# Kernel tuning notes

Measured on AMD Instinct MI355X. Metric: run time of the kernel, lower is better.

The kernel has to match this reference:

```python
import jax, jax.numpy as jnp
import numpy as np

FEATURE_SIZE = 1_000_000
EMB = 64
BATCH = 16384
ONEHOT = 26
MULTIHOT = 2
MH_LEN = 20
DENSE = 13
NN_IN = EMB * (ONEHOT + MULTIHOT) + DENSE  # 1805
UNITS = [1024, 512, 1]


def setup_inputs() -> dict:
    key = jax.random.key(0)
    ks = jax.random.split(key, 12)
    glorot = lambda k, shape: jax.random.normal(k, shape, jnp.float32) * np.sqrt(2.0 / (shape[0] + shape[-1])).astype(np.float32)
    return {
        "dense": jax.random.normal(ks[0], (BATCH, DENSE), jnp.float32),
        "onehot": jax.random.randint(ks[1], (BATCH, ONEHOT), 0, FEATURE_SIZE),
        "multihot": jax.random.randint(ks[2], (BATCH, MULTIHOT, MH_LEN), 0, FEATURE_SIZE),
        "fm_w": glorot(ks[3], (FEATURE_SIZE, 1)),
        "fm_emb": glorot(ks[4], (FEATURE_SIZE, EMB)),
        "w0": glorot(ks[5], (NN_IN, UNITS[0])),
        "b0": jnp.zeros((1,), jnp.float32),
        "w1": glorot(ks[6], (UNITS[0], UNITS[1])),
        "b1": jnp.zeros((1,), jnp.float32),
        "w2": glorot(ks[7], (UNITS[1], UNITS[2])),
        "b2": jnp.zeros((1,), jnp.float32),
    }


def reference(dense, onehot, multihot, fm_w, fm_emb, w0, b0, w1, b1, w2, b2):
    B = dense.shape[0]
    # Embedding gathers
    onehot_emb = fm_emb[onehot]                       # (B, 26, E)
    multihot_emb = fm_emb[multihot].mean(axis=2)      # (B, 2, L, E) -> (B, 2, E) mean combiner
    cat_emb = jnp.concatenate([onehot_emb, multihot_emb], axis=1)  # (B, 28, E)
    # FM 1st order (only onehot, as in original code)
    fm_1st = jnp.sum(fm_w[onehot], axis=1)            # (B, 1)
    # FM 2nd order: 0.5 * ((sum v)^2 - sum v^2)
    s = jnp.sum(cat_emb, axis=1)                      # (B, E)
    fm_2nd = 0.5 * (jnp.square(s) - jnp.sum(jnp.square(cat_emb), axis=1))
    fm_2nd = jnp.sum(fm_2nd, axis=1, keepdims=True)   # (B, 1)
    # Deep part (ReLU on every layer, incl. last, as in original)
    nn = jnp.concatenate([cat_emb.reshape(B, -1), dense], axis=1)  # (B, 1805)
    for w, b in ((w0, b0), (w1, b1), (w2, b2)):
        nn = jax.nn.relu(nn @ w + b)
    return jax.nn.sigmoid(fm_1st + fm_2nd + nn)       # (B, 1)
```

## Files before the change

### kernel.cpp

```cpp
#include <hip/hip_runtime.h>
#include <hip/hip_bf16.h>
#include <math.h>

typedef __attribute__((ext_vector_type(8))) short bf16x8;
typedef __attribute__((ext_vector_type(4))) float f32x4;

typedef void __attribute__((address_space(1))) gvoid_t;
typedef void __attribute__((address_space(3))) lvoid_t;

#define KP0   1824
#define NB    16384
#define OFF_X    0u
#define OFF_H0   59768832u
#define OFF_W0T  93323264u
#define OFF_W1T  97058816u
#define OFF_FM   98107392u

#define VMCNT(n) asm volatile("s_waitcnt vmcnt(" #n ")" ::: "memory")

__device__ __forceinline__ float bf2f(short s) {
    return __uint_as_float(((unsigned)(unsigned short)s) << 16);
}

__device__ __forceinline__ void load_lds16(const void* g, void* l) {
    __builtin_amdgcn_global_load_lds(
        (gvoid_t*)(uintptr_t)g,
        (lvoid_t*)(unsigned)(uintptr_t)l,
        16, 0, 0);
}

__global__ __launch_bounds__(256) void transpose_w(const float* __restrict__ W,
                                                   __hip_bfloat16* __restrict__ WT,
                                                   int K, int N, int KP) {
    __shared__ float tile[32][33];
    const int k0 = blockIdx.x * 32, n0 = blockIdx.y * 32;
    const int tx = threadIdx.x, ty = threadIdx.y;
    #pragma unroll
    for (int i = 0; i < 32; i += 8) {
        int k = k0 + ty + i;
        tile[ty + i][tx] = (k < K) ? W[(size_t)k * N + (n0 + tx)] : 0.f;
    }
    __syncthreads();
    #pragma unroll
    for (int i = 0; i < 32; i += 8) {
        int n = n0 + ty + i, k = k0 + tx;
        WT[(size_t)n * KP + k] = __float2bfloat16(tile[tx][ty + i]);
    }
}

__global__ __launch_bounds__(256) void gather_fm(const float* __restrict__ dense,
                                                 const int* __restrict__ onehot,
                                                 const int* __restrict__ multihot,
                                                 const float* __restrict__ fm_w,
                                                 const float* __restrict__ fm_emb,
                                                 __hip_bfloat16* __restrict__ X,
                                                 float* __restrict__ FM) {
    const int wv = threadIdx.x >> 6, lane = threadIdx.x & 63;
    const int row = blockIdx.x * 4 + wv;
    const int oh = (lane < 26) ? onehot[row * 26 + lane] : 0;
    const int mh = (lane < 40) ? multihot[row * 40 + lane] : 0;
    const float fm1 = (lane < 26) ? fm_w[oh] : 0.f;
    __hip_bfloat16* Xr = X + (size_t)row * KP0;
    float s = 0.f, sq = 0.f;
    for (int f = 0; f < 26; ++f) {
        int idx = __shfl(oh, f);
        float v = fm_emb[(size_t)idx * 64 + lane];
        s += v; sq += v * v;
        Xr[f * 64 + lane] = __float2bfloat16(v);
    }
    #pragma unroll
    for (int h = 0; h < 2; ++h) {
        float a = 0.f;
        for (int l = 0; l < 20; ++l) {
            int idx = __shfl(mh, h * 20 + l);
            a += fm_emb[(size_t)idx * 64 + lane];
        }
        float v = a * (1.f / 20.f);
        s += v; sq += v * v;
        Xr[(26 + h) * 64 + lane] = __float2bfloat16(v);
    }
    float red = 0.5f * (s * s - sq) + fm1;
    #pragma unroll
    for (int off = 32; off; off >>= 1) red += __shfl_xor(red, off);
    if (lane == 0) FM[row] = red;
    if (lane < 32) {
        float dv = (lane < 13) ? dense[row * 13 + lane] : 0.f;
        Xr[1792 + lane] = __float2bfloat16(dv);
    }
}

template<int NREP>
__global__ __launch_bounds__(512, 2) void gemm_pipe(const __hip_bfloat16* __restrict__ A,
                                                    const __hip_bfloat16* __restrict__ BT,
                                                    const float* __restrict__ bias,
                                                    __hip_bfloat16* __restrict__ C,
                                                    int M, int N, int K) {
    constexpr int BBY = NREP * 4096;
    __shared__ __align__(16) char lds[4][16384 + BBY];
    const int tid = threadIdx.x;
    const int wv = tid >> 6, lane = tid & 63;
    const int lr = lane & 15, lg = lane >> 4;
    const int wr = wv >> 2, wc = wv & 3;

    const int bid = blockIdx.x;
    const int wg = (bid & 7) * 32 + (bid >> 3);
    const int br = wg >> 2, bc = wg & 3;

    const size_t rowBytes = (size_t)K * 2;
    const char* Ab = (const char*)A + (size_t)(br * 256) * rowBytes;
    const char* Bb = (const char*)BT + (size_t)(bc * (NREP * 64)) * rowBytes;
    const int nt = K >> 5;

    auto stage = [&](int kt) {
        const int buf = kt & 3;
        const size_t kb = (size_t)kt * 64;
        #pragma unroll
        for (int i = 0; i < 2; ++i) {
            int o = i * 8192 + wv * 1024 + lane * 16;
            int row = o >> 6, slot = (o >> 4) & 3;
            int sg = slot ^ ((row >> 1) & 3);
            load_lds16(Ab + (size_t)row * rowBytes + kb + sg * 16,
                       &lds[buf][i * 8192 + wv * 1024]);
        }
        #pragma unroll
        for (int i = 0; i < NREP / 2; ++i) {
            int o = i * 8192 + wv * 1024 + lane * 16;
            int row = o >> 6, slot = (o >> 4) & 3;
            int sg = slot ^ ((row >> 1) & 3);
            load_lds16(Bb + (size_t)row * rowBytes + kb + sg * 16,
                       &lds[buf][16384 + i * 8192 + wv * 1024]);
        }
    };

    f32x4 acc[8][NREP] = {};

    stage(0); stage(1); stage(2);
    if constexpr (NREP == 4) VMCNT(8); else VMCNT(6);
    __builtin_amdgcn_s_barrier();
    __builtin_amdgcn_sched_barrier(0);

    const int swz = ((lr >> 1) & 3) << 4;
    const int aoff0 = (wr * 128 + lr) * 64 + ((lg << 4) ^ swz);
    const int boff0 = 16384 + (wc * (NREP * 16) + lr) * 64 + ((lg << 4) ^ swz);

    for (int kt = 0; kt < nt; ++kt) {
        if (kt + 3 < nt) stage(kt + 3);
        __builtin_amdgcn_sched_barrier(0);

        const char* base = lds[kt & 3];
        bf16x8 a[8], b[NREP];
        #pragma unroll
        for (int m = 0; m < 8; ++m)
            a[m] = *(const bf16x8*)(base + aoff0 + m * 1024);
        #pragma unroll
        for (int n = 0; n < NREP; ++n)
            b[n] = *(const bf16x8*)(base + boff0 + n * 1024);

        __builtin_amdgcn_s_setprio(1);
        #pragma unroll
        for (int m = 0; m < 8; ++m)
            #pragma unroll
            for (int n = 0; n < NREP; ++n)
                acc[m][n] = __builtin_amdgcn_mfma_f32_16x16x32_bf16(a[m], b[n], acc[m][n], 0, 0, 0);
        __builtin_amdgcn_s_setprio(0);

        if (kt + 1 < nt) {
            asm volatile("s_waitcnt lgkmcnt(0)" ::: "memory");
            if (kt + 3 < nt)      { if constexpr (NREP == 4) VMCNT(8); else VMCNT(6); }
            else if (kt + 2 < nt) { if constexpr (NREP == 4) VMCNT(4); else VMCNT(3); }
            else                  { VMCNT(0); }
            __builtin_amdgcn_s_barrier();
            __builtin_amdgcn_sched_barrier(0);
        }
    }

    const float bv = bias[0];
    const int rowb = br * 256 + wr * 128, colb = bc * (NREP * 64) + wc * (NREP * 16);
    #pragma unroll
    for (int m = 0; m < 8; ++m)
        #pragma unroll
        for (int n = 0; n < NREP; ++n)
            #pragma unroll
            for (int r = 0; r < 4; ++r) {
                int row = rowb + m * 16 + lg * 4 + r;
                int col = colb + n * 16 + lr;
                C[(size_t)row * N + col] = __float2bfloat16(fmaxf(acc[m][n][r] + bv, 0.f));
            }
}

__global__ __launch_bounds__(256) void final_k(const __hip_bfloat16* __restrict__ H1,
                                               const float* __restrict__ w2,
                                               const float* __restrict__ b2,
                                               const float* __restrict__ FM,
                                               float* __restrict__ out) {
    const int wv = threadIdx.x >> 6, lane = threadIdx.x & 63;
    const int row = blockIdx.x * 4 + wv;
    const bf16x8 h = *(const bf16x8*)(H1 + (size_t)row * 512 + lane * 8);
    float s = 0.f;
    #pragma unroll
    for (int j = 0; j < 8; ++j) s += bf2f(h[j]) * w2[lane * 8 + j];
    #pragma unroll
    for (int off = 32; off; off >>= 1) s += __shfl_xor(s, off);
    if (lane == 0) {
        float v = fmaxf(s + b2[0], 0.f) + FM[row];
        out[row] = 1.f / (1.f + expf(-v));
    }
}

extern "C" void kernel_launch(void* const* d_in, const int* in_sizes, int n_in,
                              void* d_out, int out_size, void* d_ws, size_t ws_size,
                              hipStream_t stream) {
    const float* dense    = (const float*)d_in[0];
    const int*   onehot   = (const int*)d_in[1];
    const int*   multihot = (const int*)d_in[2];
    const float* fm_w     = (const float*)d_in[3];
    const float* fm_emb   = (const float*)d_in[4];
    const float* w0       = (const float*)d_in[5];
    const float* b0       = (const float*)d_in[6];
    const float* w1       = (const float*)d_in[7];
    const float* b1       = (const float*)d_in[8];
    const float* w2       = (const float*)d_in[9];
    const float* b2       = (const float*)d_in[10];
    float* out = (float*)d_out;

    char* ws = (char*)d_ws;
    __hip_bfloat16* X   = (__hip_bfloat16*)(ws + OFF_X);
    __hip_bfloat16* H1  = (__hip_bfloat16*)(ws + OFF_X);
    __hip_bfloat16* H0  = (__hip_bfloat16*)(ws + OFF_H0);
    __hip_bfloat16* W0T = (__hip_bfloat16*)(ws + OFF_W0T);
    __hip_bfloat16* W1T = (__hip_bfloat16*)(ws + OFF_W1T);
    float*          FM  = (float*)(ws + OFF_FM);

    transpose_w<<<dim3(57, 32), dim3(32, 8), 0, stream>>>(w0, W0T, 1805, 1024, KP0);
    transpose_w<<<dim3(32, 16), dim3(32, 8), 0, stream>>>(w1, W1T, 1024, 512, 1024);
    gather_fm<<<NB / 4, 256, 0, stream>>>(dense, onehot, multihot, fm_w, fm_emb, X, FM);
    gemm_pipe<4><<<256, 512, 0, stream>>>(X,  W0T, b0, H0, NB, 1024, KP0);
    gemm_pipe<2><<<256, 512, 0, stream>>>(H0, W1T, b1, H1, NB, 512, 1024);
    final_k<<<NB / 4, 256, 0, stream>>>(H1, w2, b2, FM, out);
}
```

Baseline: 178.0 us.

## Restructure GEMM to 64-wide K tiles with padded LDS and interleaved staging

The GEMM kernel now uses 64-element K tiles in a double-buffered LDS layout with padded rows (144/160 bytes) instead of an XOR swizzle and a 4-deep 32-wide pipeline. Each K step is split into phases, and global-to-LDS loads for tile t+2 are interleaved between MFMA phases, with a barrier around each phase. KP0 is raised to 1856 so K is a multiple of 64, and workspace offsets and the gather padding are adjusted to match. The aim is fewer loop iterations and better overlap of loads with MFMA, at the cost of many more barriers and some extra zero-padded K work.

```diff
diff --git a/kernel.cpp b/kernel.cpp
--- a/kernel.cpp
+++ b/kernel.cpp
@@ -8,15 +8,17 @@
 typedef void __attribute__((address_space(1))) gvoid_t;
 typedef void __attribute__((address_space(3))) lvoid_t;
 
-#define KP0   1824
+#define KP0   1856
 #define NB    16384
 #define OFF_X    0u
-#define OFF_H0   59768832u
-#define OFF_W0T  93323264u
-#define OFF_W1T  97058816u
-#define OFF_FM   98107392u
+#define OFF_H0   60817408u
+#define OFF_W0T  94371840u
+#define OFF_W1T  98172928u
+#define OFF_FM   99221504u
 
 #define VMCNT(n) asm volatile("s_waitcnt vmcnt(" #n ")" ::: "memory")
+#define LGKM0()  asm volatile("s_waitcnt lgkmcnt(0)" ::: "memory")
+#define SBAR0()  __builtin_amdgcn_sched_barrier(0)
 
 __device__ __forceinline__ float bf2f(short s) {
     return __uint_as_float(((unsigned)(unsigned short)s) << 16);
@@ -83,10 +85,8 @@
     #pragma unroll
     for (int off = 32; off; off >>= 1) red += __shfl_xor(red, off);
     if (lane == 0) FM[row] = red;
-    if (lane < 32) {
-        float dv = (lane < 13) ? dense[row * 13 + lane] : 0.f;
-        Xr[1792 + lane] = __float2bfloat16(dv);
-    }
+    float dv = (lane < 13) ? dense[row * 13 + lane] : 0.f;
+    Xr[1792 + lane] = __float2bfloat16(dv);
 }
 
 template<int NREP>
@@ -95,8 +95,13 @@
                                                     const float* __restrict__ bias,
                                                     __hip_bfloat16* __restrict__ C,
                                                     int M, int N, int K) {
-    constexpr int BBY = NREP * 4096;
-    __shared__ __align__(16) char lds[4][16384 + BBY];
+    constexpr int AB   = 256 * 144;
+    constexpr int BROW = (NREP == 4) ? 144 : 160;
+    constexpr int BB   = (NREP == 4) ? 256 * 144 : 128 * 160;
+    constexpr int TOT  = AB + BB;
+    constexpr int LOADS = TOT / 8192;
+    __shared__ __align__(16) char lds[2][TOT];
+
     const int tid = threadIdx.x;
     const int wv = tid >> 6, lane = tid & 63;
     const int lr = lane & 15, lg = lane >> 4;
@@ -109,69 +114,152 @@
     const size_t rowBytes = (size_t)K * 2;
     const char* Ab = (const char*)A + (size_t)(br * 256) * rowBytes;
     const char* Bb = (const char*)BT + (size_t)(bc * (NREP * 64)) * rowBytes;
-    const int nt = K >> 5;
-
-    auto stage = [&](int kt) {
-        const int buf = kt & 3;
-        const size_t kb = (size_t)kt * 64;
-        #pragma unroll
-        for (int i = 0; i < 2; ++i) {
-            int o = i * 8192 + wv * 1024 + lane * 16;
-            int row = o >> 6, slot = (o >> 4) & 3;
-            int sg = slot ^ ((row >> 1) & 3);
-            load_lds16(Ab + (size_t)row * rowBytes + kb + sg * 16,
-                       &lds[buf][i * 8192 + wv * 1024]);
-        }
-        #pragma unroll
-        for (int i = 0; i < NREP / 2; ++i) {
-            int o = i * 8192 + wv * 1024 + lane * 16;
-            int row = o >> 6, slot = (o >> 4) & 3;
-            int sg = slot ^ ((row >> 1) & 3);
-            load_lds16(Bb + (size_t)row * rowBytes + kb + sg * 16,
-                       &lds[buf][16384 + i * 8192 + wv * 1024]);
-        }
+    const int nt = K >> 6;
+
+    auto stage_chunk = [&](int t, int i) {
+        const size_t kb = (size_t)t * 128;
+        const int o = i * 8192 + tid * 16;
+        const char* src;
+        if (o < AB) {
+            int row = o / 144, c = o % 144;
+            if (c >= 128) c = 0;
+            src = Ab + (size_t)row * rowBytes + kb + c;
+        } else {
+            int ob = o - AB;
+            int row = ob / BROW, c = ob % BROW;
+            if (c >= 128) c = 0;
+            src = Bb + (size_t)row * rowBytes + kb + c;
+        }
+        load_lds16(src, &lds[t & 1][i * 8192 + wv * 1024]);
     };
 
     f32x4 acc[8][NREP] = {};
 
-    stage(0); stage(1); stage(2);
-    if constexpr (NREP == 4) VMCNT(8); else VMCNT(6);
+    for (int i = 0; i < LOADS; ++i) stage_chunk(0, i);
+    for (int i = 0; i < LOADS; ++i) stage_chunk(1, i);
+    if constexpr (NREP == 4) VMCNT(9); else VMCNT(7);
     __builtin_amdgcn_s_barrier();
-    __builtin_amdgcn_sched_barrier(0);
-
-    const int swz = ((lr >> 1) & 3) << 4;
-    const int aoff0 = (wr * 128 + lr) * 64 + ((lg << 4) ^ swz);
-    const int boff0 = 16384 + (wc * (NREP * 16) + lr) * 64 + ((lg << 4) ^ swz);
-
-    for (int kt = 0; kt < nt; ++kt) {
-        if (kt + 3 < nt) stage(kt + 3);
-        __builtin_amdgcn_sched_barrier(0);
-
-        const char* base = lds[kt & 3];
-        bf16x8 a[8], b[NREP];
-        #pragma unroll
-        for (int m = 0; m < 8; ++m)
-            a[m] = *(const bf16x8*)(base + aoff0 + m * 1024);
-        #pragma unroll
-        for (int n = 0; n < NREP; ++n)
-            b[n] = *(const bf16x8*)(base + boff0 + n * 1024);
-
+    SBAR0();
+
+    const int aoff = (wr * 128 + lr) * 144 + lg * 16;
+    const int boff = AB + (wc * (NREP * 16) + lr) * BROW + lg * 16;
+
+    for (int t = 0; t < nt; ++t) {
+        const char* L = &lds[t & 1][0];
+        const bool st = (t + 2 < nt);
+        bf16x8 a[4][2], b[NREP][2];
+
+        #pragma unroll
+        for (int m = 0; m < 4; ++m)
+            #pragma unroll
+            for (int kk = 0; kk < 2; ++kk)
+                a[m][kk] = *(const bf16x8*)(L + aoff + m * 2304 + kk * 64);
+        #pragma unroll
+        for (int n = 0; n < 2; ++n)
+            #pragma unroll
+            for (int kk = 0; kk < 2; ++kk)
+                b[n][kk] = *(const bf16x8*)(L + boff + n * (16 * BROW) + kk * 64);
+        SBAR0();
+        __builtin_amdgcn_s_barrier();
+        LGKM0(); SBAR0();
         __builtin_amdgcn_s_setprio(1);
         #pragma unroll
-        for (int m = 0; m < 8; ++m)
-            #pragma unroll
-            for (int n = 0; n < NREP; ++n)
-                acc[m][n] = __builtin_amdgcn_mfma_f32_16x16x32_bf16(a[m], b[n], acc[m][n], 0, 0, 0);
+        for (int m = 0; m < 4; ++m)
+            #pragma unroll
+            for (int n = 0; n < 2; ++n)
+                #pragma unroll
+                for (int kk = 0; kk < 2; ++kk)
+                    acc[m][n] = __builtin_amdgcn_mfma_f32_16x16x32_bf16(a[m][kk], b[n][kk], acc[m][n], 0, 0, 0);
         __builtin_amdgcn_s_setprio(0);
-
-        if (kt + 1 < nt) {
-            asm volatile("s_waitcnt lgkmcnt(0)" ::: "memory");
-            if (kt + 3 < nt)      { if constexpr (NREP == 4) VMCNT(8); else VMCNT(6); }
-            else if (kt + 2 < nt) { if constexpr (NREP == 4) VMCNT(4); else VMCNT(3); }
-            else                  { VMCNT(0); }
+        SBAR0();
+        __builtin_amdgcn_s_barrier();
+
+        if constexpr (NREP == 4) {
+            #pragma unroll
+            for (int n = 2; n < 4; ++n)
+                #pragma unroll
+                for (int kk = 0; kk < 2; ++kk)
+                    b[n][kk] = *(const bf16x8*)(L + boff + n * (16 * BROW) + kk * 64);
+            SBAR0();
             __builtin_amdgcn_s_barrier();
-            __builtin_amdgcn_sched_barrier(0);
-        }
+            LGKM0(); SBAR0();
+            __builtin_amdgcn_s_setprio(1);
+            #pragma unroll
+            for (int m = 0; m < 4; ++m)
+                #pragma unroll
+                for (int n = 2; n < 4; ++n)
+                    #pragma unroll
+                    for (int kk = 0; kk < 2; ++kk)
+                        acc[m][n] = __builtin_amdgcn_mfma_f32_16x16x32_bf16(a[m][kk], b[n][kk], acc[m][n], 0, 0, 0);
+            __builtin_amdgcn_s_setprio(0);
+            SBAR0();
+            __builtin_amdgcn_s_barrier();
+        }
+
+        #pragma unroll
+        for (int m = 0; m < 4; ++m)
+            #pragma unroll
+            for (int kk = 0; kk < 2; ++kk)
+                a[m][kk] = *(const bf16x8*)(L + aoff + (4 + m) * 2304 + kk * 64);
+        if (st) {
+            if constexpr (NREP == 4) {
+                stage_chunk(t + 2, 5); stage_chunk(t + 2, 6);
+                stage_chunk(t + 2, 7); stage_chunk(t + 2, 8);
+            } else {
+                stage_chunk(t + 2, 5); stage_chunk(t + 2, 6);
+            }
+        }
+        SBAR0();
+        __builtin_amdgcn_s_barrier();
+        LGKM0(); SBAR0();
+        __builtin_amdgcn_s_setprio(1);
+        if constexpr (NREP == 4) {
+            #pragma unroll
+            for (int m = 0; m < 4; ++m)
+                #pragma unroll
+                for (int n = 0; n < 2; ++n)
+                    #pragma unroll
+                    for (int kk = 0; kk < 2; ++kk)
+                        acc[4 + m][n] = __builtin_amdgcn_mfma_f32_16x16x32_bf16(a[m][kk], b[n][kk], acc[4 + m][n], 0, 0, 0);
+        } else {
+            #pragma unroll
+            for (int m = 0; m < 4; ++m)
+                #pragma unroll
+                for (int kk = 0; kk < 2; ++kk)
+                    acc[4 + m][0] = __builtin_amdgcn_mfma_f32_16x16x32_bf16(a[m][kk], b[0][kk], acc[4 + m][0], 0, 0, 0);
+        }
+        __builtin_amdgcn_s_setprio(0);
+        SBAR0();
+        __builtin_amdgcn_s_barrier();
+
+        if (st) {
+            #pragma unroll
+            for (int i = 0; i < 5; ++i) stage_chunk(t + 2, i);
+        }
+        SBAR0();
+        __builtin_amdgcn_s_barrier();
+        LGKM0(); SBAR0();
+        __builtin_amdgcn_s_setprio(1);
+        if constexpr (NREP == 4) {
+            #pragma unroll
+            for (int m = 0; m < 4; ++m)
+                #pragma unroll
+                for (int n = 2; n < 4; ++n)
+                    #pragma unroll
+                    for (int kk = 0; kk < 2; ++kk)
+                        acc[4 + m][n] = __builtin_amdgcn_mfma_f32_16x16x32_bf16(a[m][kk], b[n][kk], acc[4 + m][n], 0, 0, 0);
+        } else {
+            #pragma unroll
+            for (int m = 0; m < 4; ++m)
+                #pragma unroll
+                for (int kk = 0; kk < 2; ++kk)
+                    acc[4 + m][1] = __builtin_amdgcn_mfma_f32_16x16x32_bf16(a[m][kk], b[1][kk], acc[4 + m][1], 0, 0, 0);
+        }
+        __builtin_amdgcn_s_setprio(0);
+        SBAR0();
+        if (t + 2 < nt) { if constexpr (NREP == 4) VMCNT(9); else VMCNT(7); }
+        else if (t + 1 < nt) VMCNT(0);
+        if (t + 1 < nt) __builtin_amdgcn_s_barrier();
     }
 
     const float bv = bias[0];
@@ -231,7 +319,7 @@
     __hip_bfloat16* W1T = (__hip_bfloat16*)(ws + OFF_W1T);
     float*          FM  = (float*)(ws + OFF_FM);
 
-    transpose_w<<<dim3(57, 32), dim3(32, 8), 0, stream>>>(w0, W0T, 1805, 1024, KP0);
+    transpose_w<<<dim3(58, 32), dim3(32, 8), 0, stream>>>(w0, W0T, 1805, 1024, KP0);
     transpose_w<<<dim3(32, 16), dim3(32, 8), 0, stream>>>(w1, W1T, 1024, 512, 1024);
     gather_fm<<<NB / 4, 256, 0, stream>>>(dense, onehot, multihot, fm_w, fm_emb, X, FM);
     gemm_pipe<4><<<256, 512, 0, stream>>>(X,  W0T, b0, H0, NB, 1024, KP0);
```

Result: slower. 190.3 us (+6.9%).
